# Performance work log

Measured on AMD Instinct MI355X. Metric: run time of the kernel, lower is better.

## Reference

```python
import jax, jax.numpy as jnp
import numpy as np
import math

B, D = 8192, 128
STEEPNESS = 1.0
TOPK_NEG = 10
N_SORT = TOPK_NEG + 1  # n_pos_augs - 1 + topk_neg = 1 + 10
EPS = 1e-8


def setup_inputs() -> dict:
    key = jax.random.key(0)
    k1, k2 = jax.random.split(key)
    aug1 = jax.random.normal(k1, (B, D), dtype=jnp.float32)
    aug2 = jax.random.normal(k2, (B, D), dtype=jnp.float32)
    return {"aug1": aug1, "aug2": aug2}


def _soft_sort_odd_even(x, steepness):
    """Differentiable odd-even transposition sort (diffsort, cauchy interpolation).
    x: [B, n]. Returns (sorted_x [B, n], P [B, n, n]) where sorted_x = x @ P and
    P[i, j] = relaxed probability that input element i lands at sorted position j."""
    b, n = x.shape
    P = jnp.broadcast_to(jnp.eye(n, dtype=x.dtype), (b, n, n))
    for layer in range(n):  # n layers, alternating even/odd pairs
        off = layer % 2
        idx_a = np.arange(off, n - 1, 2)
        idx_b = idx_a + 1
        a = x[:, idx_a]
        bb = x[:, idx_b]
        # cauchy CDF relaxation: alpha -> 1 when b > a (already ordered)
        alpha = jnp.arctan(steepness * (bb - a)) / math.pi + 0.5
        x = x.at[:, idx_a].set(alpha * a + (1.0 - alpha) * bb)
        x = x.at[:, idx_b].set((1.0 - alpha) * a + alpha * bb)
        Pa = P[:, :, idx_a]
        Pb = P[:, :, idx_b]
        al = alpha[:, None, :]
        P = P.at[:, :, idx_a].set(al * Pa + (1.0 - al) * Pb)
        P = P.at[:, :, idx_b].set((1.0 - al) * Pa + al * Pb)
    return x, P


def _bce(p, t):
    # torch.nn.BCELoss with log clamped at -100
    logp = jnp.clip(jnp.log(p), -100.0, None)
    log1mp = jnp.clip(jnp.log(1.0 - p), -100.0, None)
    return -jnp.mean(t * logp + (1.0 - t) * log1mp)


def _compute_loss(anchor, positive):
    anchor = anchor.astype(jnp.float32)
    positive = jax.lax.stop_gradient(positive.astype(jnp.float32))  # stop_grad=True
    # pairwise cosine similarity (dim=1)
    an = anchor / jnp.maximum(jnp.linalg.norm(anchor, axis=1, keepdims=True), EPS)
    pn = positive / jnp.maximum(jnp.linalg.norm(positive, axis=1, keepdims=True), EPS)
    pos_sims = jnp.sum(an * pn, axis=1, keepdims=True)  # [B, 1]; sort over dim=1 is a no-op
    # all-to-all cosine similarity vs detached anchors (negatives = anchor.detach())
    negs = jax.lax.stop_gradient(an)
    sim = an @ negs.T  # [B, B]
    nb = sim.shape[0]
    sim = jnp.where(jnp.eye(nb, dtype=bool), -jnp.inf, sim)  # mask self-similarity
    neg_top, _ = jax.lax.top_k(sim, TOPK_NEG)  # descending
    neg_top = neg_top[:, ::-1]                 # flip -> ascending
    sims = jnp.concatenate([neg_top, pos_sims], axis=1)  # [B, 11]
    _, P = _soft_sort_odd_even(sims, STEEPNESS)
    n = sims.shape[1]
    # perm_target = identity -> column-sum targets are first-k indicators
    p_neg = jnp.clip(jnp.sum(P[:, :, :TOPK_NEG], axis=2), 0.0, 1.0)  # [B, n]
    p_pos = jnp.clip(jnp.sum(P[:, :, TOPK_NEG:], axis=2), 0.0, 1.0)
    t_neg = jnp.broadcast_to((jnp.arange(n) < TOPK_NEG).astype(jnp.float32), (nb, n))
    t_pos = 1.0 - t_neg
    return 0.5 * (_bce(p_pos, t_pos) + _bce(p_neg, t_neg))


def reference(aug1, aug2):
    # n_augs = 2: each aug serves as anchor once, the other as the single positive
    loss1 = _compute_loss(aug1, aug2)
    loss2 = _compute_loss(aug2, aug1)
    return (loss1 + loss2) / 2.0
```

## Files before the change

### kernel.cpp

```cpp
#include <hip/hip_runtime.h>
#include <cstdint>
#include <cmath>

#define NB 8192
#define ND 128
#define CAP 64
#define NEG_INF (-__builtin_inff())

typedef __attribute__((ext_vector_type(8))) __bf16 bf16x8;
typedef __attribute__((ext_vector_type(2))) __bf16 bf16x2;
typedef __attribute__((ext_vector_type(4))) float f32x4;

__device__ __forceinline__ void insert10(float t[10], float v) {
#pragma unroll
  for (int j = 0; j < 9; ++j) t[j] = __builtin_amdgcn_fmed3f(t[j], t[j + 1], v);
  t[9] = fmaxf(t[9], v);
}
__device__ __forceinline__ void insert11(float t[11], float v) {
#pragma unroll
  for (int j = 0; j < 10; ++j) t[j] = __builtin_amdgcn_fmed3f(t[j], t[j + 1], v);
  t[10] = fmaxf(t[10], v);
}

__device__ float row_loss(float x[11]) {
  float al[55];
#pragma unroll
  for (int layer = 0; layer < 11; ++layer) {
#pragma unroll
    for (int p = 0; p < 5; ++p) {
      int ii = (layer & 1) + 2 * p;
      float av = x[ii], bv = x[ii + 1];
      float a = atanf(bv - av) * 0.3183098861837907f + 0.5f;
      al[layer * 5 + p] = a;
      float be = 1.f - a;
      x[ii] = a * av + be * bv;
      x[ii + 1] = be * av + a * bv;
    }
  }
  float v[11];
#pragma unroll
  for (int i = 0; i < 11; ++i) v[i] = 0.f;
  v[10] = 1.f;
#pragma unroll
  for (int layer = 10; layer >= 0; --layer) {
#pragma unroll
    for (int p = 0; p < 5; ++p) {
      int ii = (layer & 1) + 2 * p;
      float a = al[layer * 5 + p];
      float be = 1.f - a;
      float va = v[ii], vb = v[ii + 1];
      v[ii] = a * va + be * vb;
      v[ii + 1] = be * va + a * vb;
    }
  }
  float C = fmaxf(logf(v[10]), -100.f);
#pragma unroll
  for (int i = 0; i < 10; ++i) C += fmaxf(logf(1.f - v[i]), -100.f);
  return C;
}

__global__ __launch_bounds__(256, 4) void knorm(const float* __restrict__ aug1,
                                                const float* __restrict__ aug2,
                                                __bf16* __restrict__ an,
                                                float* __restrict__ pos,
                                                float* __restrict__ out) {
  if (blockIdx.x == 0 && threadIdx.x == 0) out[0] = 0.f;
  int wid = threadIdx.x >> 6;
  int l = threadIdx.x & 63;
  int row = blockIdx.x * 4 + wid;
  const float2* a1 = (const float2*)(aug1) + (size_t)row * 64;
  const float2* a2 = (const float2*)(aug2) + (size_t)row * 64;
  float2 v1 = a1[l], v2 = a2[l];
  float ss1 = v1.x * v1.x + v1.y * v1.y;
  float ss2 = v2.x * v2.x + v2.y * v2.y;
  float dp = v1.x * v2.x + v1.y * v2.y;
#pragma unroll
  for (int off = 1; off < 64; off <<= 1) {
    ss1 += __shfl_xor(ss1, off);
    ss2 += __shfl_xor(ss2, off);
    dp += __shfl_xor(dp, off);
  }
  float inv1 = 1.0f / fmaxf(sqrtf(ss1), 1e-8f);
  float inv2 = 1.0f / fmaxf(sqrtf(ss2), 1e-8f);
  bf16x2 o1, o2;
  o1[0] = (__bf16)(v1.x * inv1);
  o1[1] = (__bf16)(v1.y * inv1);
  o2[0] = (__bf16)(v2.x * inv2);
  o2[1] = (__bf16)(v2.y * inv2);
  ((bf16x2*)(an))[(size_t)row * 64 + l] = o1;
  ((bf16x2*)(an + (size_t)NB * ND))[(size_t)row * 64 + l] = o2;
  if (l == 0) pos[row] = dp * inv1 * inv2;
}

__device__ __forceinline__ void consume4(const f32x4* acc, float (*cand)[CAP],
                                         int* lcnt, float tau, int c) {
#pragma unroll
  for (int rb = 0; rb < 4; ++rb) {
    int rl = rb * 16 + c;
#pragma unroll
    for (int r = 0; r < 4; ++r) {
      float v = acc[rb][r];
      if (v > tau) {
        int s = atomicAdd(&lcnt[rl], 1);
        if (s < CAP) cand[rl][s] = v;
      }
    }
  }
}

__global__ __launch_bounds__(256, 3) void kgram(const __bf16* __restrict__ an_all,
                                                float* __restrict__ tk,
                                                int* __restrict__ cnth,
                                                float* __restrict__ taug) {
  int dir = blockIdx.y;
  int rowg = blockIdx.x >> 1;
  int half = blockIdx.x & 1;
  const bf16x8* an8 = (const bf16x8*)(an_all + (size_t)dir * NB * ND);
  int w = threadIdx.x >> 6;
  int l = threadIdx.x & 63;
  int q = l >> 4;
  int c = l & 15;
  int row_base = rowg * 64;
  const int col0 = half * 4096;

  __shared__ float cand[64][CAP];
  __shared__ int lcnt[64];
  __shared__ float sred[2][4];
  if (threadIdx.x < 64) lcnt[threadIdx.x] = 0;

  bf16x8 brow[4][4];
#pragma unroll
  for (int rb = 0; rb < 4; ++rb)
#pragma unroll
    for (int kc = 0; kc < 4; ++kc)
      brow[rb][kc] = an8[(size_t)(row_base + rb * 16 + c) * 16 + kc * 4 + q];

  const bf16x8* pf0 = an8 + ((size_t)(col0 + w * 16 + c) * 16 + q);
  bf16x8 a[4], a2[4];
  const f32x4 zz = {0.f, 0.f, 0.f, 0.f};
  f32x4 accA[4], accB[4];

  auto loadA = [&](int t) {
    const bf16x8* p = pf0 + (size_t)(t & 63) * 1024;
#pragma unroll
    for (int kc = 0; kc < 4; ++kc) a[kc] = p[kc * 4];
  };
  auto loadA2 = [&](int t) {
    const bf16x8* p = pf0 + (size_t)(t & 63) * 1024;
#pragma unroll
    for (int kc = 0; kc < 4; ++kc) a2[kc] = p[kc * 4];
  };
  auto mfma_tile = [&](f32x4* A, const bf16x8* src) {
#pragma unroll
    for (int rb = 0; rb < 4; ++rb)
      A[rb] = __builtin_amdgcn_mfma_f32_16x16x32_bf16(src[0], brow[rb][0], zz, 0, 0, 0);
#pragma unroll
    for (int kc = 1; kc < 4; ++kc)
#pragma unroll
      for (int rb = 0; rb < 4; ++rb)
        A[rb] = __builtin_amdgcn_mfma_f32_16x16x32_bf16(src[kc], brow[rb][kc], A[rb], 0, 0, 0);
  };

  loadA(0);
  mfma_tile(accA, a);
  loadA2(1);
  bool diag0 = (row_base == col0);
  int cq0 = col0 + w * 16 + q * 4;
  float s1 = 0.f, s2 = 0.f;
#pragma unroll
  for (int rb = 0; rb < 4; ++rb) {
    int myrow = row_base + rb * 16 + c;
#pragma unroll
    for (int r = 0; r < 4; ++r) {
      float v = accA[rb][r];
      v = (diag0 && (cq0 + r == myrow)) ? 0.f : v;
      s1 += v;
      s2 = fmaf(v, v, s2);
    }
  }
#pragma unroll
  for (int off = 1; off < 64; off <<= 1) {
    s1 += __shfl_xor(s1, off);
    s2 += __shfl_xor(s2, off);
  }
  if (l == 0) { sred[0][w] = s1; sred[1][w] = s2; }
  __syncthreads();
  float n = diag0 ? 4032.f : 4096.f;
  float ts1 = sred[0][0] + sred[0][1] + sred[0][2] + sred[0][3];
  float ts2 = sred[1][0] + sred[1][1] + sred[1][2] + sred[1][3];
  float mu = ts1 / n;
  float sig = sqrtf(fmaxf(ts2 / n - mu * mu, 0.f));
  float tau = mu + 2.5f * sig;
  if (threadIdx.x == 0) taug[(dir * 128 + rowg) * 2 + half] = tau;
  consume4(accA, cand, lcnt, tau, c);

  mfma_tile(accA, a2);
  loadA(2);
  for (int t = 2; t < 64; t += 2) {
    mfma_tile(accB, a);
    loadA2(t + 1);
    consume4(accA, cand, lcnt, tau, c);
    mfma_tile(accA, a2);
    loadA(t + 2);
    consume4(accB, cand, lcnt, tau, c);
  }
  consume4(accA, cand, lcnt, tau, c);

  __syncthreads();
  if (threadIdx.x < 64) {
    int rl = threadIdx.x;
    int cc = lcnt[rl];
    float t11[11];
#pragma unroll
    for (int j = 0; j < 11; ++j) t11[j] = NEG_INF;
    int m = cc < CAP ? cc : CAP;
    for (int i = 0; i < m; ++i) {
      float v = cand[rl][i];
      if (v > t11[0]) insert11(t11, v);
    }
    bool diagq = (row_base >= col0) && (row_base < col0 + 4096);
    float* o = tk + ((size_t)(dir * NB + row_base + rl) * 2 + half) * 10;
    if (diagq) {
#pragma unroll
      for (int j = 0; j < 10; ++j) o[j] = t11[j];
    } else {
#pragma unroll
      for (int j = 0; j < 10; ++j) o[j] = t11[j + 1];
    }
    cnth[(dir * NB + row_base + rl) * 2 + half] = cc;
  }
}

__global__ __launch_bounds__(64, 1) void ksort(const float* __restrict__ tk,
                                               const float* __restrict__ pos,
                                               const int* __restrict__ cnth,
                                               const float* __restrict__ taug,
                                               const __bf16* __restrict__ an_all,
                                               float* __restrict__ out) {
  int tid = blockIdx.x * 64 + threadIdx.x;
  int dir = tid >> 13;
  int row = tid & (NB - 1);
  int lane = threadIdx.x;

  const float* A = tk + (size_t)(dir * NB + row) * 20;
  float s10[10];
#pragma unroll
  for (int j = 0; j < 10; ++j) s10[j] = A[j];
#pragma unroll
  for (int j = 0; j < 10; ++j) {
    float v = A[10 + j];
    if (v > s10[0]) insert10(s10, v);
  }
  int rowg = row >> 6;
  float tmax = fmaxf(taug[(dir * 128 + rowg) * 2], taug[(dir * 128 + rowg) * 2 + 1]);
  int2 cc2 = ((const int2*)cnth)[dir * NB + row];
  bool ok = (cc2.x <= CAP) && (cc2.y <= CAP) && (s10[0] >= tmax);

  float C = 0.f;
  if (ok) {
    float x[11];
#pragma unroll
    for (int j = 0; j < 10; ++j) x[j] = s10[j];
    x[10] = pos[row];
    C = row_loss(x);
  }
#pragma unroll
  for (int off = 1; off < 64; off <<= 1) C += __shfl_xor(C, off);
  if (lane == 0) atomicAdd(out, C * (-1.f / (2.f * (float)NB * 11.f)));

  unsigned long long bad = __ballot(!ok);
  if (bad == 0ull) return;
  __shared__ float rv[128];
  __shared__ float lst[64][10];
  const __bf16* an = an_all + (size_t)dir * NB * ND;
  while (bad) {
    int b = __ffsll((long long)bad) - 1;
    bad &= bad - 1;
    int brow = (blockIdx.x * 64 + b) & (NB - 1);
    bf16x2 pr = ((const bf16x2*)an)[(size_t)brow * 64 + lane];
    rv[lane * 2] = (float)pr[0];
    rv[lane * 2 + 1] = (float)pr[1];
    __syncthreads();
    float t10[10];
#pragma unroll
    for (int j = 0; j < 10; ++j) t10[j] = NEG_INF;
    for (int i = 0; i < 128; ++i) {
      int col = lane + i * 64;
      if (col == brow) continue;
      const bf16x8* cp = (const bf16x8*)(an + (size_t)col * ND);
      float d = 0.f;
#pragma unroll
      for (int k = 0; k < 16; ++k) {
        bf16x8 p = cp[k];
#pragma unroll
        for (int e = 0; e < 8; ++e) d = fmaf(rv[k * 8 + e], (float)p[e], d);
      }
      if (d > t10[0]) insert10(t10, d);
    }
#pragma unroll
    for (int j = 0; j < 10; ++j) lst[lane][j] = t10[j];
    __syncthreads();
    if (lane == 0) {
      float cur[10];
#pragma unroll
      for (int j = 0; j < 10; ++j) cur[j] = lst[0][j];
      for (int s = 1; s < 64; ++s)
        for (int j = 0; j < 10; ++j) {
          float v = lst[s][j];
          if (v > cur[0]) insert10(cur, v);
        }
      float x[11];
#pragma unroll
      for (int j = 0; j < 10; ++j) x[j] = cur[j];
      x[10] = pos[brow];
      atomicAdd(out, row_loss(x) * (-1.f / (2.f * (float)NB * 11.f)));
    }
    __syncthreads();
  }
}

extern "C" void kernel_launch(void* const* d_in, const int* in_sizes, int n_in,
                              void* d_out, int out_size, void* d_ws, size_t ws_size,
                              hipStream_t stream) {
  const float* aug1 = (const float*)d_in[0];
  const float* aug2 = (const float*)d_in[1];
  char* w = (char*)d_ws;
  __bf16* an = (__bf16*)w;
  float* pos = (float*)(w + (size_t)4 * 1024 * 1024);
  float* tk = pos + NB;
  int* cnth = (int*)(tk + (size_t)2 * NB * 20);
  float* taug = (float*)(cnth + 2 * NB * 2);

  knorm<<<dim3(NB / 4), dim3(256), 0, stream>>>(aug1, aug2, an, pos, (float*)d_out);
  kgram<<<dim3(256, 2), dim3(256), 0, stream>>>(an, tk, cnth, taug);
  ksort<<<dim3(2 * NB / 64), dim3(64), 0, stream>>>(tk, pos, cnth, taug, an, (float*)d_out);
}
```

Before: 139.7 us.

## Stage column panels through LDS with async global_load_lds double buffering

Replaces the direct per-lane global loads of column tiles with async global_load_lds copies into a swizzled, double-buffered LDS panel. Each wave reads its MFMA fragments back from LDS and syncs once per iteration. The cand array is padded to 65 columns to reduce bank conflicts, and the launch-bounds occupancy hint drops from 3 to 2. In exchange, the loop loses the register ping-pong of two accumulators and adds an LDS round trip plus a block barrier on every tile, so latency hiding may get worse.

New measurement: 157.6 us. 12.8% more time.

```diff
diff --git a/kernel.cpp b/kernel.cpp
--- a/kernel.cpp
+++ b/kernel.cpp
@@ -5,6 +5,7 @@
 #define NB 8192
 #define ND 128
 #define CAP 64
+#define CAPP 65
 #define NEG_INF (-__builtin_inff())
 
 typedef __attribute__((ext_vector_type(8))) __bf16 bf16x8;
@@ -92,7 +93,7 @@
   if (l == 0) pos[row] = dp * inv1 * inv2;
 }
 
-__device__ __forceinline__ void consume4(const f32x4* acc, float (*cand)[CAP],
+__device__ __forceinline__ void consume4(const f32x4* acc, float (*cand)[CAPP],
                                          int* lcnt, float tau, int c) {
 #pragma unroll
   for (int rb = 0; rb < 4; ++rb) {
@@ -108,14 +109,15 @@
   }
 }
 
-__global__ __launch_bounds__(256, 3) void kgram(const __bf16* __restrict__ an_all,
+__global__ __launch_bounds__(256, 2) void kgram(const __bf16* __restrict__ an_all,
                                                 float* __restrict__ tk,
                                                 int* __restrict__ cnth,
                                                 float* __restrict__ taug) {
   int dir = blockIdx.y;
   int rowg = blockIdx.x >> 1;
   int half = blockIdx.x & 1;
-  const bf16x8* an8 = (const bf16x8*)(an_all + (size_t)dir * NB * ND);
+  const __bf16* an = an_all + (size_t)dir * NB * ND;
+  const bf16x8* an8 = (const bf16x8*)an;
   int w = threadIdx.x >> 6;
   int l = threadIdx.x & 63;
   int q = l >> 4;
@@ -123,7 +125,8 @@
   int row_base = rowg * 64;
   const int col0 = half * 4096;
 
-  __shared__ float cand[64][CAP];
+  __shared__ char sbuf[2][16384];
+  __shared__ float cand[64][CAPP];
   __shared__ int lcnt[64];
   __shared__ float sred[2][4];
   if (threadIdx.x < 64) lcnt[threadIdx.x] = 0;
@@ -135,21 +138,32 @@
     for (int kc = 0; kc < 4; ++kc)
       brow[rb][kc] = an8[(size_t)(row_base + rb * 16 + c) * 16 + kc * 4 + q];
 
-  const bf16x8* pf0 = an8 + ((size_t)(col0 + w * 16 + c) * 16 + q);
-  bf16x8 a[4], a2[4];
+  const char* panel = (const char*)an + (size_t)col0 * 256;
+  const int seE = (w * 16 + q) * 256 + ((c ^ q) << 4);
+  const int seO = (w * 16 + q) * 256 + (((c ^ q) ^ 4) << 4);
+  auto stage = [&](int buf, int t) {
+    const char* tb = panel + (size_t)t * 16384;
+    char* db = &sbuf[buf][w * 4096];
+#pragma unroll
+    for (int k = 0; k < 4; ++k) {
+      const char* src = tb + ((k & 1) ? seO : seE) + k * 1024;
+      __builtin_amdgcn_global_load_lds(
+          (const __attribute__((address_space(1))) void*)src,
+          (__attribute__((address_space(3))) void*)(db + k * 1024), 16, 0, 0);
+    }
+  };
+
+  int rdo[4];
+#pragma unroll
+  for (int kc = 0; kc < 4; ++kc)
+    rdo[kc] = (w * 16 + c) * 256 + ((((kc * 4 + q) ^ (c & 7))) << 4);
+  auto readfr = [&](int buf, bf16x8* a) {
+    const char* bp = &sbuf[buf][0];
+#pragma unroll
+    for (int kc = 0; kc < 4; ++kc) a[kc] = *(const bf16x8*)(bp + rdo[kc]);
+  };
+
   const f32x4 zz = {0.f, 0.f, 0.f, 0.f};
-  f32x4 accA[4], accB[4];
-
-  auto loadA = [&](int t) {
-    const bf16x8* p = pf0 + (size_t)(t & 63) * 1024;
-#pragma unroll
-    for (int kc = 0; kc < 4; ++kc) a[kc] = p[kc * 4];
-  };
-  auto loadA2 = [&](int t) {
-    const bf16x8* p = pf0 + (size_t)(t & 63) * 1024;
-#pragma unroll
-    for (int kc = 0; kc < 4; ++kc) a2[kc] = p[kc * 4];
-  };
   auto mfma_tile = [&](f32x4* A, const bf16x8* src) {
 #pragma unroll
     for (int rb = 0; rb < 4; ++rb)
@@ -161,9 +175,13 @@
         A[rb] = __builtin_amdgcn_mfma_f32_16x16x32_bf16(src[kc], brow[rb][kc], A[rb], 0, 0, 0);
   };
 
-  loadA(0);
-  mfma_tile(accA, a);
-  loadA2(1);
+  stage(0, 0);
+  __syncthreads();
+  stage(1, 1);
+  bf16x8 a[4];
+  f32x4 acc[4];
+  readfr(0, a);
+  mfma_tile(acc, a);
   bool diag0 = (row_base == col0);
   int cq0 = col0 + w * 16 + q * 4;
   float s1 = 0.f, s2 = 0.f;
@@ -172,7 +190,7 @@
     int myrow = row_base + rb * 16 + c;
 #pragma unroll
     for (int r = 0; r < 4; ++r) {
-      float v = accA[rb][r];
+      float v = acc[rb][r];
       v = (diag0 && (cq0 + r == myrow)) ? 0.f : v;
       s1 += v;
       s2 = fmaf(v, v, s2);
@@ -192,21 +210,17 @@
   float sig = sqrtf(fmaxf(ts2 / n - mu * mu, 0.f));
   float tau = mu + 2.5f * sig;
   if (threadIdx.x == 0) taug[(dir * 128 + rowg) * 2 + half] = tau;
-  consume4(accA, cand, lcnt, tau, c);
-
-  mfma_tile(accA, a2);
-  loadA(2);
-  for (int t = 2; t < 64; t += 2) {
-    mfma_tile(accB, a);
-    loadA2(t + 1);
-    consume4(accA, cand, lcnt, tau, c);
-    mfma_tile(accA, a2);
-    loadA(t + 2);
-    consume4(accB, cand, lcnt, tau, c);
-  }
-  consume4(accA, cand, lcnt, tau, c);
-
-  __syncthreads();
+  consume4(acc, cand, lcnt, tau, c);
+
+  for (int t = 1; t < 64; ++t) {
+    int cur = t & 1;
+    if (t < 63) stage(cur ^ 1, t + 1);
+    readfr(cur, a);
+    mfma_tile(acc, a);
+    consume4(acc, cand, lcnt, tau, c);
+    __syncthreads();
+  }
+
   if (threadIdx.x < 64) {
     int rl = threadIdx.x;
     int cc = lcnt[rl];
```
